# Kernel optimization log

Measured on AMD Instinct MI355X. Metric: run time of the kernel, lower is better.

## Reference

```python
import jax, jax.numpy as jnp
import numpy as np

WS = 5       # window_size
SHIFT = 2    # shift_size
NH = 3       # num_heads (hardcoded in module)
EPS = 1e-5   # LayerNorm eps (torch default)

B, H, W, C = 4, 400, 400, 48


def _window_partition(x, ws):
    b, h, w, c = x.shape
    x = x.reshape(b, h // ws, ws, w // ws, ws, c).transpose(0, 1, 3, 2, 4, 5)
    return x.reshape(-1, ws * ws, c)  # [B*nH*nW, ws*ws, C]


def _window_reverse(x, ws, h, w):
    bn = x.shape[0] // ((h // ws) * (w // ws))
    x = x.reshape(bn, h // ws, w // ws, ws, ws, -1).transpose(0, 1, 3, 2, 4, 5)
    return x.reshape(bn, h, w, -1)


def _qkv_branch(win, qkv_w, qkv_b, ln_g, ln_b):
    # Linear -> LayerNorm(last dim) -> Softmax over window-position axis (dim 1)
    y = win @ qkv_w + qkv_b                      # [B_, N, 3C]
    mu = jnp.mean(y, axis=-1, keepdims=True)
    var = jnp.mean((y - mu) ** 2, axis=-1, keepdims=True)
    y = (y - mu) * jax.lax.rsqrt(var + EPS) * ln_g + ln_b
    y = jax.nn.softmax(y, axis=1)                # nn.Softmax(1)
    b_, n, _ = y.shape
    y = y.reshape(b_, n, 3, NH, C // NH).transpose(2, 0, 3, 1, 4)  # [3, B_, h, N, d]
    return y[0], y[1], y[2]


def setup_inputs() -> dict:
    key = jax.random.key(0)
    ks = jax.random.split(key, 4)
    lr_patch = jax.random.normal(ks[0], (B, H, W, C), jnp.float32)
    ref_patch = jax.random.normal(ks[1], (B, H, W, C), jnp.float32)
    qkv_w = jax.random.normal(ks[2], (C, 3 * C), jnp.float32) * (1.0 / np.sqrt(C))
    qkv_b = jax.random.normal(ks[3], (3 * C,), jnp.float32) * 0.01
    ln_g = jnp.ones((3 * C,), jnp.float32)
    ln_b = jnp.zeros((3 * C,), jnp.float32)
    return {"lr_patch": lr_patch, "ref_patch": ref_patch, "qkv_w": qkv_w,
            "qkv_b": qkv_b, "ln_g": ln_g, "ln_b": ln_b}


def reference(lr_patch, ref_patch, qkv_w, qkv_b, ln_g, ln_b):
    # cyclic shift
    s_lr = jnp.roll(lr_patch, shift=(-SHIFT, -SHIFT), axis=(1, 2))
    s_ref = jnp.roll(ref_patch, shift=(-SHIFT, -SHIFT), axis=(1, 2))

    lr_w = _window_partition(s_lr, WS)    # [B_, N=25, C]
    ref_w = _window_partition(s_ref, WS)

    q_lr, k_lr, v_lr = _qkv_branch(lr_w, qkv_w, qkv_b, ln_g, ln_b)
    q_ref, k_ref, v_ref = _qkv_branch(ref_w, qkv_w, qkv_b, ln_g, ln_b)

    # dual cross-attention (no scaling / no second softmax, as in source)
    attn1 = jnp.einsum('bhnd,bhmd->bhnm', q_lr, k_ref)   # [B_, h, N, N]
    attn2 = jnp.einsum('bhnd,bhmd->bhnm', q_ref, k_lr)
    x = jnp.einsum('bhnm,bhmd->bhnd', attn1, v_ref)
    x = jnp.einsum('bhnm,bhmd->bhnd', attn2, x)

    b_, _, n, _ = x.shape
    x = x.transpose(0, 2, 1, 3).reshape(b_, n, C)        # [B_, N, C]
    x = x.reshape(-1, WS, WS, C)

    x = _window_reverse(x, WS, H, W)
    x = jnp.roll(x, shift=(SHIFT, SHIFT), axis=(1, 2))
    return (x, ref_patch)
```

## Files before the change

### kernel.cpp

```cpp
#include <hip/hip_runtime.h>
#include <hip/hip_bf16.h>

typedef __hip_bfloat16 hbf16;
typedef unsigned short u16t;
typedef __attribute__((ext_vector_type(8))) short bf16x8;
typedef __attribute__((ext_vector_type(4))) float f32x4;

#define WSZ 5
#define CC 48
#define C3 144
#define HDIM 400
#define NWH 80
#define SH 2
#define ITERS 4
#define YROWS 57
#define YW 152
#define WTW 56
#define PW 40

__device__ __forceinline__ u16t f2b(float x) {
    union { hbf16 h; u16t u; } c;
    c.h = __float2bfloat16(x);
    return c.u;
}
__device__ __forceinline__ unsigned pk2(float lo, float hi) {
    return ((unsigned)f2b(hi) << 16) | f2b(lo);
}

__global__ __launch_bounds__(512, 4) void swin_mfma5(
    const float* __restrict__ lr, const float* __restrict__ ref,
    const float* __restrict__ qkv_w, const float* __restrict__ qkv_b,
    const float* __restrict__ ln_g, const float* __restrict__ ln_b,
    float* __restrict__ out, float* __restrict__ out1)
{
    __shared__ __align__(16) u16t s_wT[C3 * WTW];
    __shared__ __align__(16) u16t s_y[2][YROWS * YW];
    __shared__ __align__(16) u16t s_P[2][3 * 32 * PW];
    __shared__ __align__(16) u16t s_x1T[2][3 * 16 * PW];
    __shared__ __align__(16) float s_ln[2][4][16][4];
    __shared__ __align__(16) float s_gb[3 * C3];

    const int tid = threadIdx.x;
    const int wave = tid >> 6, lane = tid & 63;
    const int lm = lane & 15, g = lane >> 4;
    const int wh = wave >> 2;
    const int w4 = wave & 3;
    const int br = w4 >> 1, jh = w4 & 1;
    const int T0 = jh ? 4 : 0;

    for (int i = tid; i < CC * C3; i += 512) {
        int c = i / C3, j = i % C3;
        s_wT[j * WTW + c] = f2b(qkv_w[i]);
    }
    for (int i = tid; i < C3; i += 512) {
        s_gb[i] = qkv_b[i];
        s_gb[C3 + i] = ln_g[i];
        s_gb[2 * C3 + i] = ln_b[i];
    }
    for (int i = tid; i < 7 * YW; i += 512) {
        s_y[0][25 * YW + i] = 0;
        s_y[1][25 * YW + i] = 0;
    }
    __syncthreads();

    const bf16x8 z8 = {0, 0, 0, 0, 0, 0, 0, 0};
    const f32x4  z4 = {0.f, 0.f, 0.f, 0.f};
    const float* xsrc = br ? ref : lr;

    for (int it = 0; it < ITERS; ++it) {
        const int wid = blockIdx.x * (2 * ITERS) + it * 2 + wh;
        const int bb = wid / (NWH * NWH);
        const int rr = wid % (NWH * NWH);
        const int bh = rr / NWH, bw = rr % NWH;

        bf16x8 xa[2], xb[2];
        #pragma unroll
        for (int s2 = 0; s2 < 2; ++s2) {
            int row = 16 * s2 + lm;
            int wi = row / WSZ, wj = row % WSZ;
            int hh = bh * WSZ + wi + SH; if (hh >= HDIM) hh -= HDIM;
            int ww = bw * WSZ + wj + SH; if (ww >= HDIM) ww -= HDIM;
            const float4* p4 = reinterpret_cast<const float4*>(
                xsrc + ((size_t)(bb * HDIM + hh) * HDIM + ww) * CC);
            float4 u = p4[2 * g], v = p4[2 * g + 1];
            bf16x8 t;
            t[0] = f2b(u.x); t[1] = f2b(u.y); t[2] = f2b(u.z); t[3] = f2b(u.w);
            t[4] = f2b(v.x); t[5] = f2b(v.y); t[6] = f2b(v.z); t[7] = f2b(v.w);
            xa[s2] = t;
            float4 u2, v2;
            if (g < 2) {
                u2 = p4[8 + 2 * g]; v2 = p4[9 + 2 * g];
                bf16x8 t2;
                t2[0] = f2b(u2.x); t2[1] = f2b(u2.y); t2[2] = f2b(u2.z); t2[3] = f2b(u2.w);
                t2[4] = f2b(v2.x); t2[5] = f2b(v2.y); t2[6] = f2b(v2.z); t2[7] = f2b(v2.w);
                xb[s2] = t2;
            } else xb[s2] = z8;
            if (w4 == 3 && row < 25) {
                float4* o1 = reinterpret_cast<float4*>(
                    out1 + ((size_t)(bb * HDIM + hh) * HDIM + ww) * CC);
                o1[2 * g] = u; o1[2 * g + 1] = v;
                if (g < 2) { o1[8 + 2 * g] = u2; o1[9 + 2 * g] = v2; }
            }
        }

        f32x4 acc[5][2];
        #pragma unroll
        for (int tt = 0; tt < 5; ++tt) {
            const int t = T0 + tt;
            bf16x8 w1 = *reinterpret_cast<const bf16x8*>(&s_wT[(16 * t + lm) * WTW + 8 * g]);
            bf16x8 w2 = *reinterpret_cast<const bf16x8*>(&s_wT[(16 * t + lm) * WTW + 32 + 8 * (g & 1)]);
            f32x4 bv = *reinterpret_cast<const f32x4*>(&s_gb[16 * t + 4 * g]);
            #pragma unroll
            for (int s2 = 0; s2 < 2; ++s2) {
                f32x4 a = bv;
                a = __builtin_amdgcn_mfma_f32_16x16x32_bf16(w1, xa[s2], a, 0, 0, 0);
                a = __builtin_amdgcn_mfma_f32_16x16x32_bf16(w2, xb[s2], a, 0, 0, 0);
                acc[tt][s2] = a;
            }
        }

        float s0 = 0.f, q0 = 0.f, s1 = 0.f, q1 = 0.f;
        #pragma unroll
        for (int tt = 0; tt < 5; ++tt) {
            if (jh == 0 || tt > 0) {
                #pragma unroll
                for (int r2 = 0; r2 < 4; ++r2) {
                    float va = acc[tt][0][r2]; s0 += va; q0 += va * va;
                    float vb = acc[tt][1][r2]; s1 += vb; q1 += vb * vb;
                }
            }
        }
        s0 += __shfl_xor(s0, 16); s0 += __shfl_xor(s0, 32);
        q0 += __shfl_xor(q0, 16); q0 += __shfl_xor(q0, 32);
        s1 += __shfl_xor(s1, 16); s1 += __shfl_xor(s1, 32);
        q1 += __shfl_xor(q1, 16); q1 += __shfl_xor(q1, 32);
        if (lane < 16) {
            float4 w4v = make_float4(s0, q0, s1, q1);
            *reinterpret_cast<float4*>(&s_ln[wh][w4][lm][0]) = w4v;
        }
        __syncthreads();
        {
            float4 p = *reinterpret_cast<const float4*>(&s_ln[wh][w4 ^ 1][lm][0]);
            float S0 = s0 + p.x, Q0 = q0 + p.y, S1 = s1 + p.z, Q1 = q1 + p.w;
            float mu0 = S0 * (1.f / 144.f);
            float rs0 = rsqrtf(Q0 * (1.f / 144.f) - mu0 * mu0 + 1e-5f);
            float mu1 = S1 * (1.f / 144.f);
            float rs1 = rsqrtf(Q1 * (1.f / 144.f) - mu1 * mu1 + 1e-5f);
            #pragma unroll
            for (int tt = 0; tt < 5; ++tt) {
                const int t = T0 + tt;
                f32x4 gv = *reinterpret_cast<const f32x4*>(&s_gb[C3 + 16 * t + 4 * g]);
                f32x4 bv2 = *reinterpret_cast<const f32x4*>(&s_gb[2 * C3 + 16 * t + 4 * g]);
                #pragma unroll
                for (int r2 = 0; r2 < 4; ++r2) {
                    acc[tt][0][r2] = (acc[tt][0][r2] - mu0) * rs0 * gv[r2] + bv2[r2];
                    acc[tt][1][r2] = (acc[tt][1][r2] - mu1) * rs1 * gv[r2] + bv2[r2];
                }
            }
        }

        #pragma unroll
        for (int tt = 0; tt < 5; ++tt) {
            const int t = T0 + tt;
            float pa[4], pb[4];
            #pragma unroll
            for (int r2 = 0; r2 < 4; ++r2) {
                float va = acc[tt][0][r2];
                float vb = (lm < 9) ? acc[tt][1][r2] : -1e30f;
                float ea = __expf(va), eb = __expf(vb);
                float ss = ea + eb;
                ss += __shfl_xor(ss, 1); ss += __shfl_xor(ss, 2);
                ss += __shfl_xor(ss, 4); ss += __shfl_xor(ss, 8);
                float inv = __builtin_amdgcn_rcpf(ss);
                pa[r2] = ea * inv; pb[r2] = eb * inv;
            }
            int colw = 16 * t + 4 * g;
            uint2 wv;
            wv.x = pk2(pa[0], pa[1]); wv.y = pk2(pa[2], pa[3]);
            *reinterpret_cast<uint2*>(&s_y[wh][(32 * br + lm) * YW + colw]) = wv;
            if (lm < 9) {
                wv.x = pk2(pb[0], pb[1]); wv.y = pk2(pb[2], pb[3]);
                *reinterpret_cast<uint2*>(&s_y[wh][(32 * br + 16 + lm) * YW + colw]) = wv;
            }
        }
        __syncthreads();

        if (w4 < 3) {
            const int h = w4;
            const int ko = 8 * (g & 1);
            const bool gok = (g < 2);
            const bool lok = (lm < 9);
            const u16t* Y = s_y[wh];
            u16t* Ph = &s_P[wh][h * 32 * PW];
            u16t* Xh = &s_x1T[wh][h * 16 * PW];
            bf16x8 ka0 = gok ? *reinterpret_cast<const bf16x8*>(&Y[(32 + lm) * YW + CC + 16 * h + ko]) : z8;
            bf16x8 ka1 = (gok && lok) ? *reinterpret_cast<const bf16x8*>(&Y[(48 + lm) * YW + CC + 16 * h + ko]) : z8;
            bf16x8 qb0 = *reinterpret_cast<const bf16x8*>(&Y[lm * YW + 16 * h + ko]);
            bf16x8 qb1 = *reinterpret_cast<const bf16x8*>(&Y[(16 + lm) * YW + 16 * h + ko]);
            f32x4 p00 = __builtin_amdgcn_mfma_f32_16x16x32_bf16(ka0, qb0, z4, 0, 0, 0);
            f32x4 p01 = __builtin_amdgcn_mfma_f32_16x16x32_bf16(ka0, qb1, z4, 0, 0, 0);
            f32x4 p10 = __builtin_amdgcn_mfma_f32_16x16x32_bf16(ka1, qb0, z4, 0, 0, 0);
            f32x4 p11 = __builtin_amdgcn_mfma_f32_16x16x32_bf16(ka1, qb1, z4, 0, 0, 0);
            uint2 wv;
            wv.x = pk2(p00[0], p00[1]); wv.y = pk2(p00[2], p00[3]);
            *reinterpret_cast<uint2*>(&Ph[lm * PW + 4 * g]) = wv;
            wv.x = pk2(p01[0], p01[1]); wv.y = pk2(p01[2], p01[3]);
            *reinterpret_cast<uint2*>(&Ph[(16 + lm) * PW + 4 * g]) = wv;
            wv.x = pk2(p10[0], p10[1]); wv.y = pk2(p10[2], p10[3]);
            *reinterpret_cast<uint2*>(&Ph[lm * PW + 16 + 4 * g]) = wv;
            wv.x = pk2(p11[0], p11[1]); wv.y = pk2(p11[2], p11[3]);
            *reinterpret_cast<uint2*>(&Ph[(16 + lm) * PW + 16 + 4 * g]) = wv;
            bf16x8 vfr;
            #pragma unroll
            for (int j = 0; j < 8; ++j) {
                int m = 8 * g + j;
                vfr[j] = (m < 25) ? (short)Y[(32 + m) * YW + 96 + 16 * h + lm] : (short)0;
            }
            bf16x8 a0 = *reinterpret_cast<const bf16x8*>(&Ph[lm * PW + 8 * g]);
            bf16x8 a1 = *reinterpret_cast<const bf16x8*>(&Ph[(16 + lm) * PW + 8 * g]);
            f32x4 x10 = __builtin_amdgcn_mfma_f32_16x16x32_bf16(a0, vfr, z4, 0, 0, 0);
            f32x4 x11 = __builtin_amdgcn_mfma_f32_16x16x32_bf16(a1, vfr, z4, 0, 0, 0);
            wv.x = pk2(x10[0], x10[1]); wv.y = pk2(x10[2], x10[3]);
            *reinterpret_cast<uint2*>(&Xh[lm * PW + 4 * g]) = wv;
            wv.x = pk2(x11[0], x11[1]); wv.y = pk2(x11[2], x11[3]);
            *reinterpret_cast<uint2*>(&Xh[lm * PW + 16 + 4 * g]) = wv;
            bf16x8 kb0 = gok ? *reinterpret_cast<const bf16x8*>(&Y[lm * YW + CC + 16 * h + ko]) : z8;
            bf16x8 kb1 = gok ? *reinterpret_cast<const bf16x8*>(&Y[(16 + lm) * YW + CC + 16 * h + ko]) : z8;
            bf16x8 qc0 = *reinterpret_cast<const bf16x8*>(&Y[(32 + lm) * YW + 16 * h + ko]);
            bf16x8 qc1 = lok ? *reinterpret_cast<const bf16x8*>(&Y[(48 + lm) * YW + 16 * h + ko]) : z8;
            p00 = __builtin_amdgcn_mfma_f32_16x16x32_bf16(kb0, qc0, z4, 0, 0, 0);
            p01 = __builtin_amdgcn_mfma_f32_16x16x32_bf16(kb0, qc1, z4, 0, 0, 0);
            p10 = __builtin_amdgcn_mfma_f32_16x16x32_bf16(kb1, qc0, z4, 0, 0, 0);
            p11 = __builtin_amdgcn_mfma_f32_16x16x32_bf16(kb1, qc1, z4, 0, 0, 0);
            wv.x = pk2(p00[0], p00[1]); wv.y = pk2(p00[2], p00[3]);
            *reinterpret_cast<uint2*>(&Ph[lm * PW + 4 * g]) = wv;
            wv.x = pk2(p01[0], p01[1]); wv.y = pk2(p01[2], p01[3]);
            *reinterpret_cast<uint2*>(&Ph[(16 + lm) * PW + 4 * g]) = wv;
            wv.x = pk2(p10[0], p10[1]); wv.y = pk2(p10[2], p10[3]);
            *reinterpret_cast<uint2*>(&Ph[lm * PW + 16 + 4 * g]) = wv;
            wv.x = pk2(p11[0], p11[1]); wv.y = pk2(p11[2], p11[3]);
            *reinterpret_cast<uint2*>(&Ph[(16 + lm) * PW + 16 + 4 * g]) = wv;
            bf16x8 xv = *reinterpret_cast<const bf16x8*>(&Xh[lm * PW + 8 * g]);
            bf16x8 pb0 = *reinterpret_cast<const bf16x8*>(&Ph[lm * PW + 8 * g]);
            bf16x8 pb1 = *reinterpret_cast<const bf16x8*>(&Ph[(16 + lm) * PW + 8 * g]);
            f32x4 o0 = __builtin_amdgcn_mfma_f32_16x16x32_bf16(xv, pb0, z4, 0, 0, 0);
            f32x4 o1v = __builtin_amdgcn_mfma_f32_16x16x32_bf16(xv, pb1, z4, 0, 0, 0);
            #pragma unroll
            for (int nt = 0; nt < 2; ++nt) {
                int n2 = 16 * nt + lm;
                if (n2 < 25) {
                    f32x4 ov = nt ? o1v : o0;
                    int wi2 = n2 / WSZ, wj2 = n2 % WSZ;
                    int oh = bh * WSZ + wi2 + SH; if (oh >= HDIM) oh -= HDIM;
                    int ow = bw * WSZ + wj2 + SH; if (ow >= HDIM) ow -= HDIM;
                    float4 o = make_float4(ov[0], ov[1], ov[2], ov[3]);
                    *reinterpret_cast<float4*>(
                        &out[((size_t)(bb * HDIM + oh) * HDIM + ow) * CC + 16 * h + 4 * g]) = o;
                }
            }
        }
    }
}

extern "C" void kernel_launch(void* const* d_in, const int* in_sizes, int n_in,
                              void* d_out, int out_size, void* d_ws, size_t ws_size,
                              hipStream_t stream) {
    const float* lr    = (const float*)d_in[0];
    const float* ref   = (const float*)d_in[1];
    const float* qkv_w = (const float*)d_in[2];
    const float* qkv_b = (const float*)d_in[3];
    const float* ln_g  = (const float*)d_in[4];
    const float* ln_b  = (const float*)d_in[5];
    float* out = (float*)d_out;
    float* out1 = out + (size_t)out_size / 2;

    const int n_blocks = 4 * NWH * NWH / (2 * ITERS);
    swin_mfma5<<<n_blocks, 512, 0, stream>>>(lr, ref, qkv_w, qkv_b, ln_g, ln_b, out, out1);
}
```

Baseline: 311.2 us.

## Prefetch next window's inputs into registers and use DPP for softmax reduction

```diff
diff --git a/kernel.cpp b/kernel.cpp
--- a/kernel.cpp
+++ b/kernel.cpp
@@ -26,8 +26,20 @@
 __device__ __forceinline__ unsigned pk2(float lo, float hi) {
     return ((unsigned)f2b(hi) << 16) | f2b(lo);
 }
-
-__global__ __launch_bounds__(512, 4) void swin_mfma5(
+__device__ __forceinline__ float dpp_add16(float x) {
+    int t;
+    t = __builtin_amdgcn_update_dpp(0, __float_as_int(x), 0xB1, 0xF, 0xF, true);
+    x += __int_as_float(t);
+    t = __builtin_amdgcn_update_dpp(0, __float_as_int(x), 0x4E, 0xF, 0xF, true);
+    x += __int_as_float(t);
+    t = __builtin_amdgcn_update_dpp(0, __float_as_int(x), 0x141, 0xF, 0xF, true);
+    x += __int_as_float(t);
+    t = __builtin_amdgcn_update_dpp(0, __float_as_int(x), 0x140, 0xF, 0xF, true);
+    x += __int_as_float(t);
+    return x;
+}
+
+__global__ __launch_bounds__(512, 4) void swin_mfma6(
     const float* __restrict__ lr, const float* __restrict__ ref,
     const float* __restrict__ qkv_w, const float* __restrict__ qkv_b,
     const float* __restrict__ ln_g, const float* __restrict__ ln_b,
@@ -47,6 +59,7 @@
     const int w4 = wave & 3;
     const int br = w4 >> 1, jh = w4 & 1;
     const int T0 = jh ? 4 : 0;
+    const bool gok = (g < 2);
 
     for (int i = tid; i < CC * C3; i += 512) {
         int c = i / C3, j = i % C3;
@@ -67,39 +80,57 @@
     const f32x4  z4 = {0.f, 0.f, 0.f, 0.f};
     const float* xsrc = br ? ref : lr;
 
-    for (int it = 0; it < ITERS; ++it) {
-        const int wid = blockIdx.x * (2 * ITERS) + it * 2 + wh;
-        const int bb = wid / (NWH * NWH);
+    float4 ra[2], rb[2], rc[2], rd[2];
+    int bb_n, bh_n, bw_n;
+
+    auto issue_loads = [&](int it2) {
+        const int wid = blockIdx.x * (2 * ITERS) + it2 * 2 + wh;
+        bb_n = wid / (NWH * NWH);
         const int rr = wid % (NWH * NWH);
-        const int bh = rr / NWH, bw = rr % NWH;
-
-        bf16x8 xa[2], xb[2];
+        bh_n = rr / NWH; bw_n = rr % NWH;
         #pragma unroll
         for (int s2 = 0; s2 < 2; ++s2) {
             int row = 16 * s2 + lm;
             int wi = row / WSZ, wj = row % WSZ;
-            int hh = bh * WSZ + wi + SH; if (hh >= HDIM) hh -= HDIM;
-            int ww = bw * WSZ + wj + SH; if (ww >= HDIM) ww -= HDIM;
+            int hh = bh_n * WSZ + wi + SH; if (hh >= HDIM) hh -= HDIM;
+            int ww = bw_n * WSZ + wj + SH; if (ww >= HDIM) ww -= HDIM;
             const float4* p4 = reinterpret_cast<const float4*>(
-                xsrc + ((size_t)(bb * HDIM + hh) * HDIM + ww) * CC);
-            float4 u = p4[2 * g], v = p4[2 * g + 1];
+                xsrc + ((size_t)(bb_n * HDIM + hh) * HDIM + ww) * CC);
+            ra[s2] = p4[2 * g];
+            rb[s2] = p4[2 * g + 1];
+            if (gok) { rc[s2] = p4[8 + 2 * g]; rd[s2] = p4[9 + 2 * g]; }
+        }
+    };
+
+    issue_loads(0);
+
+    for (int it = 0; it < ITERS; ++it) {
+        const int bb = bb_n, bh = bh_n, bw = bw_n;
+
+        bf16x8 xa[2], xb[2];
+        #pragma unroll
+        for (int s2 = 0; s2 < 2; ++s2) {
+            float4 u = ra[s2], v = rb[s2];
             bf16x8 t;
             t[0] = f2b(u.x); t[1] = f2b(u.y); t[2] = f2b(u.z); t[3] = f2b(u.w);
             t[4] = f2b(v.x); t[5] = f2b(v.y); t[6] = f2b(v.z); t[7] = f2b(v.w);
             xa[s2] = t;
-            float4 u2, v2;
-            if (g < 2) {
-                u2 = p4[8 + 2 * g]; v2 = p4[9 + 2 * g];
+            if (gok) {
+                float4 u2 = rc[s2], v2 = rd[s2];
                 bf16x8 t2;
                 t2[0] = f2b(u2.x); t2[1] = f2b(u2.y); t2[2] = f2b(u2.z); t2[3] = f2b(u2.w);
                 t2[4] = f2b(v2.x); t2[5] = f2b(v2.y); t2[6] = f2b(v2.z); t2[7] = f2b(v2.w);
                 xb[s2] = t2;
             } else xb[s2] = z8;
+            int row = 16 * s2 + lm;
             if (w4 == 3 && row < 25) {
+                int wi = row / WSZ, wj = row % WSZ;
+                int hh = bh * WSZ + wi + SH; if (hh >= HDIM) hh -= HDIM;
+                int ww = bw * WSZ + wj + SH; if (ww >= HDIM) ww -= HDIM;
                 float4* o1 = reinterpret_cast<float4*>(
                     out1 + ((size_t)(bb * HDIM + hh) * HDIM + ww) * CC);
-                o1[2 * g] = u; o1[2 * g + 1] = v;
-                if (g < 2) { o1[8 + 2 * g] = u2; o1[9 + 2 * g] = v2; }
+                o1[2 * g] = ra[s2]; o1[2 * g + 1] = rb[s2];
+                if (gok) { o1[8 + 2 * g] = rc[s2]; o1[9 + 2 * g] = rd[s2]; }
             }
         }
 
@@ -168,9 +199,7 @@
                 float va = acc[tt][0][r2];
                 float vb = (lm < 9) ? acc[tt][1][r2] : -1e30f;
                 float ea = __expf(va), eb = __expf(vb);
-                float ss = ea + eb;
-                ss += __shfl_xor(ss, 1); ss += __shfl_xor(ss, 2);
-                ss += __shfl_xor(ss, 4); ss += __shfl_xor(ss, 8);
+                float ss = dpp_add16(ea + eb);
                 float inv = __builtin_amdgcn_rcpf(ss);
                 pa[r2] = ea * inv; pb[r2] = eb * inv;
             }
@@ -185,10 +214,11 @@
         }
         __syncthreads();
 
+        if (it + 1 < ITERS) issue_loads(it + 1);
+
         if (w4 < 3) {
             const int h = w4;
             const int ko = 8 * (g & 1);
-            const bool gok = (g < 2);
             const bool lok = (lm < 9);
             const u16t* Y = s_y[wh];
             u16t* Ph = &s_P[wh][h * 32 * PW];
@@ -275,5 +305,5 @@
     float* out1 = out + (size_t)out_size / 2;
 
     const int n_blocks = 4 * NWH * NWH / (2 * ITERS);
-    swin_mfma5<<<n_blocks, 512, 0, stream>>>(lr, ref, qkv_w, qkv_b, ln_g, ln_b, out, out1);
-}
+    swin_mfma6<<<n_blocks, 512, 0, stream>>>(lr, ref, qkv_w, qkv_b, ln_g, ln_b, out, out1);
+}
```

Result: slower. 459.0 us (+47.5%).
